# Kernel tuning notes

Measured on AMD Instinct MI355X. Metric: run time of the kernel, lower is better.

## Reference

```python
import jax, jax.numpy as jnp
import numpy as np

B, CIN, L = 16, 256, 2048
HID, G, M = 512, 2, 512
LP = L // 2  # pooled length == hidden_length of patterns
BETA = 1.0


def setup_inputs() -> dict:
    key = jax.random.key(0)
    k = jax.random.split(key, 6)
    x = jax.random.normal(k[0], (B, CIN, L), dtype=jnp.float32)
    # ChannelPool: Conv1d(256 -> 512, kernel=1, groups=2): weight [512, 128, 1]
    w1 = jax.random.normal(k[1], (HID, CIN // G, 1), dtype=jnp.float32) * 0.05
    b1 = jax.random.normal(k[2], (HID,), dtype=jnp.float32) * 0.01
    # StatePattern memory bank: [num_memories, hidden_length]
    patterns = jax.random.normal(k[3], (M, LP), dtype=jnp.float32) * 0.02
    # Unpool: ConvTranspose1d(512 -> 256, kernel=2, stride=2, groups=2):
    # torch weight layout [in_channels, out_channels//groups, kernel] = [512, 128, 2]
    wT = jax.random.normal(k[4], (HID, CIN // G, 2), dtype=jnp.float32) * 0.05
    bT = jax.random.normal(k[5], (CIN,), dtype=jnp.float32) * 0.01
    RZ = jnp.array(0.1, dtype=jnp.float32)
    return {"x": x, "w1": w1, "b1": b1, "patterns": patterns, "wT": wT, "bT": bT, "RZ": RZ}


def reference(x, w1, b1, patterns, wT, bT, RZ):
    identity = x
    # --- grouped 1x1 conv (ChannelPool) ---
    # split channels into G groups: x [B,G,CIN/G,L], w [G,HID/G,CIN/G]
    xg = x.reshape(B, G, CIN // G, L)
    wg = w1[:, :, 0].reshape(G, HID // G, CIN // G)
    h = jnp.einsum('bgil,goi->bgol', xg, wg).reshape(B, HID, L) + b1[None, :, None]
    h = jax.nn.relu(h)  # act; norm1/dropout are identity (norm=False, eval)
    # --- MaxPool1d(kernel=2, stride=2) ---
    h = h.reshape(B, HID, LP, 2).max(axis=-1)  # [B, HID, LP]
    # --- Hopfield retrieval: softmax(beta * x @ P^T) @ P ---
    scores = jnp.einsum('bcl,ml->bcm', BETA * h, patterns)  # [B, HID, M]
    attn = jax.nn.softmax(scores, axis=-1)
    h = jnp.einsum('bcm,ml->bcl', attn, patterns)  # [B, HID, LP]
    # --- grouped ConvTranspose1d(k=2, s=2) ---
    hg = h.reshape(B, G, HID // G, LP)
    wtg = wT.reshape(G, HID // G, CIN // G, 2)
    y = jnp.einsum('bgil,giok->bgolk', hg, wtg)  # [B,G,CIN/G,LP,2]
    y = y.reshape(B, CIN, L) + bT[None, :, None]
    y = jax.nn.relu(y)  # act; norm2/dropout identity
    return identity + RZ * y
```

## Files before the change

kernel.cpp:

```cpp
#include <hip/hip_runtime.h>

#define NB 16
#define NCIN 256
#define NL 2048
#define NHID 512
#define NM 512
#define NLP 1024

typedef short bf16x8 __attribute__((ext_vector_type(8)));
typedef unsigned short u16x8 __attribute__((ext_vector_type(8)));
typedef float f32x4 __attribute__((ext_vector_type(4)));
typedef __attribute__((address_space(1))) const unsigned int gas_u32;
typedef __attribute__((address_space(3))) unsigned int las_u32;

__device__ __forceinline__ unsigned short f2bf(float f) {
    unsigned int u = __builtin_bit_cast(unsigned int, f);
    return (unsigned short)((u + 0x7FFFu + ((u >> 16) & 1u)) >> 16);
}
__device__ __forceinline__ float bf2f(unsigned short u) {
    return __builtin_bit_cast(float, ((unsigned int)u) << 16);
}

__global__ __launch_bounds__(512) void k_front(
    const float* __restrict__ x, const float* __restrict__ w1,
    const float* __restrict__ b1, const float* __restrict__ P,
    const float* __restrict__ wT, unsigned short* __restrict__ hb,
    unsigned short* __restrict__ Pb, unsigned short* __restrict__ Ptb,
    unsigned short* __restrict__ wTt)
{
    __shared__ __align__(16) unsigned short smem[66560];
    const int bb = blockIdx.x;
    const int t = threadIdx.x;

    if (bb >= 512) {
        if (bb < 640) {
            unsigned short (*tbuf)[65] = (unsigned short (*)[65])smem;
            const int pb = bb - 512;
            const int mt = pb >> 4, lt = pb & 15;
            for (int i = t; i < 4096; i += 512) {
                const int r = i >> 6, c = i & 63;
                const unsigned short v = f2bf(P[(size_t)(mt * 64 + r) * 1024 + lt * 64 + c]);
                Pb[(size_t)(mt * 64 + r) * 1024 + lt * 64 + c] = v;
                tbuf[c][r] = v;
            }
            __syncthreads();
            for (int i = t; i < 4096; i += 512) {
                const int r = i >> 6, c = i & 63;
                Ptb[(size_t)(lt * 64 + r) * 512 + mt * 64 + c] = tbuf[r][c];
            }
        } else {
            const int t5 = (bb - 640) * 512 + t;
            const int g = t5 >> 16, ok = (t5 >> 8) & 255, i = t5 & 255;
            wTt[t5] = f2bf(wT[(size_t)(g * 256 + i) * 256 + ok]);
        }
        return;
    }

    const int g  = bb & 1;
    const int rt = bb >> 1;
    const int r0 = rt * 128;
    const int b  = r0 >> 11, l0 = r0 & 2047;

    unsigned short* T   = smem;
    unsigned short* Asl = smem + 17408;
    unsigned short* Bsl = smem + 33792;
    unsigned short* epi = smem;

    #pragma unroll
    for (int i3 = 0; i3 < 8; ++i3) {
        const int idx = i3 * 512 + t;
        const int ch = idx >> 5, f4 = idx & 31;
        const float4 v = *(const float4*)(x + ((size_t)(b * 256 + g * 128 + ch)) * 2048 + l0 + f4 * 4);
        ushort4 u;
        u.x = f2bf(v.x); u.y = f2bf(v.y); u.z = f2bf(v.z); u.w = f2bf(v.w);
        *(ushort4*)(T + ch * 136 + f4 * 4) = u;
    }
    #pragma unroll
    for (int i5 = 0; i5 < 16; ++i5) {
        const int idx = i5 * 512 + t;
        const int o = idx >> 5, f4 = idx & 31;
        const float4 v = *(const float4*)(w1 + ((size_t)(g * 256 + o)) * 128 + f4 * 4);
        ushort4 u;
        u.x = f2bf(v.x); u.y = f2bf(v.y); u.z = f2bf(v.z); u.w = f2bf(v.w);
        *(ushort4*)(Bsl + o * 128 + f4 * 4) = u;
    }
    __syncthreads();
    #pragma unroll
    for (int i4 = 0; i4 < 4; ++i4) {
        const int idx = i4 * 512 + t;
        const int ch = idx & 127, lo = idx >> 7;
        const u16x8 v = *(const u16x8*)(T + ch * 136 + lo * 8);
        #pragma unroll
        for (int u2 = 0; u2 < 8; ++u2)
            Asl[(lo * 8 + u2) * 128 + ch] = v[u2];
    }
    __syncthreads();

    const int lane = t & 63, wave = t >> 6;
    const int wm = wave & 1, wn = wave >> 1;
    const int q = lane >> 4, lm = lane & 15;

    f32x4 acc[4][4];
    #pragma unroll
    for (int i = 0; i < 4; ++i)
        #pragma unroll
        for (int j = 0; j < 4; ++j)
            #pragma unroll
            for (int r = 0; r < 4; ++r) acc[i][j][r] = 0.f;

    #pragma unroll
    for (int kc = 0; kc < 4; ++kc) {
        bf16x8 af[4], bf[4];
        #pragma unroll
        for (int i = 0; i < 4; ++i)
            af[i] = *(const bf16x8*)(Asl + (wm * 64 + i * 16 + lm) * 128 + kc * 32 + q * 8);
        #pragma unroll
        for (int j = 0; j < 4; ++j)
            bf[j] = *(const bf16x8*)(Bsl + (wn * 64 + j * 16 + lm) * 128 + kc * 32 + q * 8);
        #pragma unroll
        for (int i = 0; i < 4; ++i)
            #pragma unroll
            for (int j = 0; j < 4; ++j)
                acc[i][j] = __builtin_amdgcn_mfma_f32_16x16x32_bf16(af[i], bf[j], acc[i][j], 0, 0, 0);
    }
    __syncthreads();

    #pragma unroll
    for (int j = 0; j < 4; ++j) {
        const int col = wn * 64 + j * 16 + lm;
        const float bias = b1[g * 256 + col];
        #pragma unroll
        for (int i = 0; i < 4; ++i) {
            const float p0 = fmaxf(fmaxf(acc[i][j][0], acc[i][j][1]) + bias, 0.f);
            const float p1 = fmaxf(fmaxf(acc[i][j][2], acc[i][j][3]) + bias, 0.f);
            const int lp_loc = wm * 32 + i * 8 + q * 2;
            ushort2 u; u.x = f2bf(p0); u.y = f2bf(p1);
            *(ushort2*)(epi + col * 72 + lp_loc) = u;
        }
    }
    __syncthreads();
    const int c_loc = t >> 1, half = t & 1;
    unsigned short* dst = hb + ((size_t)(b * 512 + g * 256 + c_loc)) * 1024 + (l0 >> 1) + half * 32;
    #pragma unroll
    for (int u = 0; u < 4; ++u)
        *(u16x8*)(dst + u * 8) = *(const u16x8*)(epi + c_loc * 72 + half * 32 + u * 8);
}

__global__ __launch_bounds__(512) void k_hop(
    const unsigned short* __restrict__ hb, const unsigned short* __restrict__ Pb,
    const unsigned short* __restrict__ Ptb, unsigned short* __restrict__ h2T)
{
    __shared__ __align__(16) unsigned short smem[51712];
    unsigned short* Sbuf = smem;
    unsigned short* Asl  = smem + 16896;
    unsigned short* Bsl  = smem + 16896 + 2048;
    unsigned short* Bsl2 = smem + 16896;

    const int t = threadIdx.x;
    const int r0 = blockIdx.x * 32;
    const int b = r0 >> 9, c0 = r0 & 511;
    const int lane = t & 63, wave = t >> 6;
    const int q = lane >> 4, lm = lane & 15;

    f32x4 acc1[2][4];
    #pragma unroll
    for (int i = 0; i < 2; ++i)
        #pragma unroll
        for (int j = 0; j < 4; ++j)
            #pragma unroll
            for (int r = 0; r < 4; ++r) acc1[i][j][r] = 0.f;

    for (int kc0 = 0; kc0 < 1024; kc0 += 64) {
        if (t < 256) {
            const int e = t * 8;
            const int row = e >> 6, col = e & 63;
            const unsigned short* ga = hb + (size_t)(r0 + row) * 1024 + kc0 + col;
            __builtin_amdgcn_global_load_lds((gas_u32*)ga, (las_u32*)(Asl + e), 16, 0, 0);
        }
        #pragma unroll
        for (int i2 = 0; i2 < 8; ++i2) {
            const int e = (i2 * 512 + t) * 8;
            const int row = e >> 6, col = e & 63;
            const unsigned short* gb = Pb + (size_t)row * 1024 + kc0 + col;
            __builtin_amdgcn_global_load_lds((gas_u32*)gb, (las_u32*)(Bsl + e), 16, 0, 0);
        }
        __syncthreads();
        #pragma unroll
        for (int kk = 0; kk < 2; ++kk) {
            bf16x8 af[2], bf[4];
            #pragma unroll
            for (int i = 0; i < 2; ++i)
                af[i] = *(const bf16x8*)(Asl + (i * 16 + lm) * 64 + kk * 32 + q * 8);
            #pragma unroll
            for (int j = 0; j < 4; ++j)
                bf[j] = *(const bf16x8*)(Bsl + (wave * 64 + j * 16 + lm) * 64 + kk * 32 + q * 8);
            #pragma unroll
            for (int i = 0; i < 2; ++i)
                #pragma unroll
                for (int j = 0; j < 4; ++j)
                    acc1[i][j] = __builtin_amdgcn_mfma_f32_16x16x32_bf16(af[i], bf[j], acc1[i][j], 0, 0, 0);
        }
        __syncthreads();
    }

    #pragma unroll
    for (int i = 0; i < 2; ++i)
        #pragma unroll
        for (int j = 0; j < 4; ++j)
            #pragma unroll
            for (int r = 0; r < 4; ++r)
                Sbuf[(i * 16 + q * 4 + r) * 528 + wave * 64 + j * 16 + lm] = f2bf(acc1[i][j][r]);
    __syncthreads();

    {
        const int rw = t >> 4, sl = t & 15;
        u16x8 sv[4];
        #pragma unroll
        for (int u = 0; u < 4; ++u)
            sv[u] = *(const u16x8*)(Sbuf + rw * 528 + sl * 32 + u * 8);
        float mx = -3.0e38f;
        #pragma unroll
        for (int u = 0; u < 4; ++u)
            #pragma unroll
            for (int j = 0; j < 8; ++j) mx = fmaxf(mx, bf2f(sv[u][j]));
        #pragma unroll
        for (int off = 1; off < 16; off <<= 1) mx = fmaxf(mx, __shfl_xor(mx, off));
        float vv[32];
        float sum = 0.f;
        #pragma unroll
        for (int u = 0; u < 4; ++u)
            #pragma unroll
            for (int j = 0; j < 8; ++j) {
                const float e = __expf(bf2f(sv[u][j]) - mx);
                vv[u * 8 + j] = e; sum += e;
            }
        #pragma unroll
        for (int off = 1; off < 16; off <<= 1) sum += __shfl_xor(sum, off);
        const float inv = 1.f / sum;
        #pragma unroll
        for (int u = 0; u < 4; ++u) {
            u16x8 ov;
            #pragma unroll
            for (int j = 0; j < 8; ++j) ov[j] = f2bf(vv[u * 8 + j] * inv);
            *(u16x8*)(Sbuf + rw * 528 + sl * 32 + u * 8) = ov;
        }
    }
    __syncthreads();

    bf16x8 a[2][16];
    #pragma unroll
    for (int i = 0; i < 2; ++i)
        #pragma unroll
        for (int kx = 0; kx < 16; ++kx)
            a[i][kx] = *(const bf16x8*)(Sbuf + (i * 16 + lm) * 528 + kx * 32 + q * 8);

    for (int lpc = 0; lpc < 4; ++lpc) {
        const int lp0c = lpc * 256;
        f32x4 acc2[2][2];
        #pragma unroll
        for (int i = 0; i < 2; ++i)
            #pragma unroll
            for (int j = 0; j < 2; ++j)
                #pragma unroll
                for (int r = 0; r < 4; ++r) acc2[i][j][r] = 0.f;

        for (int kc0 = 0; kc0 < 4; ++kc0) {
            #pragma unroll
            for (int i2 = 0; i2 < 8; ++i2) {
                const int e = (i2 * 512 + t) * 8;
                const int row = e >> 7, col = e & 127;
                const unsigned short* gb = Ptb + (size_t)(lp0c + row) * 512 + kc0 * 128 + col;
                __builtin_amdgcn_global_load_lds((gas_u32*)gb, (las_u32*)(Bsl2 + e), 16, 0, 0);
            }
            __syncthreads();
            #pragma unroll
            for (int kk = 0; kk < 4; ++kk) {
                const int kx = kc0 * 4 + kk;
                bf16x8 bf2[2];
                #pragma unroll
                for (int j = 0; j < 2; ++j)
                    bf2[j] = *(const bf16x8*)(Bsl2 + (wave * 32 + j * 16 + lm) * 128 + kk * 32 + q * 8);
                #pragma unroll
                for (int i = 0; i < 2; ++i)
                    #pragma unroll
                    for (int j = 0; j < 2; ++j)
                        acc2[i][j] = __builtin_amdgcn_mfma_f32_16x16x32_bf16(a[i][kx], bf2[j], acc2[i][j], 0, 0, 0);
            }
            __syncthreads();
        }
        #pragma unroll
        for (int i = 0; i < 2; ++i)
            #pragma unroll
            for (int j = 0; j < 2; ++j) {
                const int lp = lp0c + wave * 32 + j * 16 + lm;
                ushort4 u;
                u.x = f2bf(acc2[i][j][0]); u.y = f2bf(acc2[i][j][1]);
                u.z = f2bf(acc2[i][j][2]); u.w = f2bf(acc2[i][j][3]);
                *(ushort4*)(h2T + ((size_t)b * 1024 + lp) * 512 + c0 + i * 16 + q * 4) = u;
            }
    }
}

__global__ __launch_bounds__(256) void k4_gemm(
    const unsigned short* __restrict__ h2T, const unsigned short* __restrict__ wTt,
    const float* __restrict__ bT, const float* __restrict__ x,
    const float* __restrict__ RZ, float* __restrict__ out)
{
    const int nt = blockIdx.x & 1;
    const int g  = (blockIdx.x >> 1) & 1;
    const int rt = blockIdx.x >> 2;
    const int r0 = rt * 128;
    const int b  = r0 >> 10, lp0 = r0 & 1023;

    __shared__ __align__(16) char smem[65536];
    unsigned short* Asl = (unsigned short*)smem;
    unsigned short* Bsl = Asl + 128 * 64;
    float* epi = (float*)smem;

    const int t = threadIdx.x;
    const int lane = t & 63;
    const int wave = t >> 6;
    const int wm = wave & 1, wn = wave >> 1;
    const int q = lane >> 4, lm = lane & 15;

    f32x4 acc[4][4];
    #pragma unroll
    for (int i = 0; i < 4; ++i)
        #pragma unroll
        for (int j = 0; j < 4; ++j)
            #pragma unroll
            for (int r = 0; r < 4; ++r) acc[i][j][r] = 0.f;

    for (int k0 = 0; k0 < 256; k0 += 64) {
        #pragma unroll
        for (int rd = 0; rd < 4; ++rd) {
            const int e = rd * 2048 + t * 8;
            const int row = e >> 6, col = e & 63;
            const unsigned short* ga = h2T + (size_t)(r0 + row) * 512 + g * 256 + k0 + col;
            __builtin_amdgcn_global_load_lds((gas_u32*)ga, (las_u32*)(Asl + e), 16, 0, 0);
            const unsigned short* gb = wTt + (size_t)g * 65536 + (size_t)(nt * 128 + row) * 256 + k0 + col;
            __builtin_amdgcn_global_load_lds((gas_u32*)gb, (las_u32*)(Bsl + e), 16, 0, 0);
        }
        __syncthreads();
        #pragma unroll
        for (int kk = 0; kk < 2; ++kk) {
            bf16x8 af[4], bf[4];
            #pragma unroll
            for (int i = 0; i < 4; ++i)
                af[i] = *(const bf16x8*)(Asl + (wm * 64 + i * 16 + lm) * 64 + kk * 32 + q * 8);
            #pragma unroll
            for (int j = 0; j < 4; ++j)
                bf[j] = *(const bf16x8*)(Bsl + (wn * 64 + j * 16 + lm) * 64 + kk * 32 + q * 8);
            #pragma unroll
            for (int i = 0; i < 4; ++i)
                #pragma unroll
                for (int j = 0; j < 4; ++j)
                    acc[i][j] = __builtin_amdgcn_mfma_f32_16x16x32_bf16(af[i], bf[j], acc[i][j], 0, 0, 0);
        }
        __syncthreads();
    }

    #pragma unroll
    for (int j = 0; j < 4; ++j) {
        const int col_blk = wn * 64 + j * 16 + lm;
        const int o_l = col_blk >> 1, kk2 = col_blk & 1;
        #pragma unroll
        for (int i = 0; i < 4; ++i) {
            #pragma unroll
            for (int r = 0; r < 4; ++r) {
                const int row_l = wm * 64 + i * 16 + q * 4 + r;
                const int l_l = 2 * row_l + kk2;
                const int chunk = ((l_l >> 2) + o_l) & 63;
                epi[o_l * 256 + chunk * 4 + (l_l & 3)] = acc[i][j][r];
            }
        }
    }
    __syncthreads();
    const int row = t >> 2, quad = t & 3;
    const int c = g * 128 + nt * 64 + row;
    const float bias = bT[c];
    const float rz = RZ[0];
    const size_t gbase = ((size_t)(b * 256 + c)) * 2048 + 2 * lp0 + quad * 64;
    #pragma unroll
    for (int k = 0; k < 16; ++k) {
        const int chunk_phys = (quad * 16 + k + row) & 63;
        const float4 v = *(const float4*)(epi + row * 256 + chunk_phys * 4);
        const float4 xv = *(const float4*)(x + gbase + k * 4);
        float4 o;
        o.x = xv.x + rz * fmaxf(v.x + bias, 0.f);
        o.y = xv.y + rz * fmaxf(v.y + bias, 0.f);
        o.z = xv.z + rz * fmaxf(v.z + bias, 0.f);
        o.w = xv.w + rz * fmaxf(v.w + bias, 0.f);
        *(float4*)(out + gbase + k * 4) = o;
    }
}

extern "C" void kernel_launch(void* const* d_in, const int* in_sizes, int n_in,
                              void* d_out, int out_size, void* d_ws, size_t ws_size,
                              hipStream_t stream) {
    (void)in_sizes; (void)n_in; (void)out_size; (void)ws_size;
    const float* x  = (const float*)d_in[0];
    const float* w1 = (const float*)d_in[1];
    const float* b1 = (const float*)d_in[2];
    const float* P  = (const float*)d_in[3];
    const float* wT = (const float*)d_in[4];
    const float* bT = (const float*)d_in[5];
    const float* RZ = (const float*)d_in[6];
    float* out = (float*)d_out;

    char* ws = (char*)d_ws;
    unsigned short* hb  = (unsigned short*)ws;
    unsigned short* h2T = (unsigned short*)(ws + (16u << 20));
    unsigned short* Pb  = (unsigned short*)(ws + (32u << 20));
    unsigned short* Ptb = (unsigned short*)(ws + (33u << 20));
    unsigned short* wTt = (unsigned short*)(ws + (34u << 20));

    hipLaunchKernelGGL(k_front, dim3(896), dim3(512), 0, stream,
                       x, w1, b1, P, wT, hb, Pb, Ptb, wTt);
    hipLaunchKernelGGL(k_hop,   dim3(256), dim3(512), 0, stream, hb, Pb, Ptb, h2T);
    hipLaunchKernelGGL(k4_gemm, dim3(512), dim3(256), 0, stream, h2T, wTt, bT, x, RZ, out);
}
```

Measured before the change: 201.2 us.

## Split fused Hopfield kernel into score GEMM and softmax-fused retrieval GEMM

```diff
diff --git a/kernel.cpp b/kernel.cpp
--- a/kernel.cpp
+++ b/kernel.cpp
@@ -146,159 +146,165 @@
         *(u16x8*)(dst + u * 8) = *(const u16x8*)(epi + c_loc * 72 + half * 32 + u * 8);
 }
 
-__global__ __launch_bounds__(512) void k_hop(
-    const unsigned short* __restrict__ hb, const unsigned short* __restrict__ Pb,
-    const unsigned short* __restrict__ Ptb, unsigned short* __restrict__ h2T)
+__global__ __launch_bounds__(512, 2) void gemm_sc(
+    const unsigned short* __restrict__ A, const unsigned short* __restrict__ B,
+    unsigned short* __restrict__ Sb)
 {
-    __shared__ __align__(16) unsigned short smem[51712];
-    unsigned short* Sbuf = smem;
-    unsigned short* Asl  = smem + 16896;
-    unsigned short* Bsl  = smem + 16896 + 2048;
-    unsigned short* Bsl2 = smem + 16896;
+    const int nt = blockIdx.x & 3;
+    const int rt = blockIdx.x >> 2;
+    const int r0 = rt * 128, n0 = nt * 128;
+
+    __shared__ unsigned short Asl[128 * 64];
+    __shared__ unsigned short Bsl[128 * 64];
 
     const int t = threadIdx.x;
-    const int r0 = blockIdx.x * 32;
-    const int b = r0 >> 9, c0 = r0 & 511;
-    const int lane = t & 63, wave = t >> 6;
+    const int lane = t & 63;
+    const int wave = t >> 6;
+    const int wm = wave & 1, wn = wave >> 1;
     const int q = lane >> 4, lm = lane & 15;
 
-    f32x4 acc1[2][4];
-    #pragma unroll
-    for (int i = 0; i < 2; ++i)
-        #pragma unroll
-        for (int j = 0; j < 4; ++j)
-            #pragma unroll
-            for (int r = 0; r < 4; ++r) acc1[i][j][r] = 0.f;
-
-    for (int kc0 = 0; kc0 < 1024; kc0 += 64) {
-        if (t < 256) {
-            const int e = t * 8;
+    f32x4 acc[4][2];
+    #pragma unroll
+    for (int i = 0; i < 4; ++i)
+        #pragma unroll
+        for (int j = 0; j < 2; ++j)
+            #pragma unroll
+            for (int r = 0; r < 4; ++r) acc[i][j][r] = 0.f;
+
+    for (int k0 = 0; k0 < 1024; k0 += 64) {
+        #pragma unroll
+        for (int rd = 0; rd < 2; ++rd) {
+            const int e = rd * 4096 + t * 8;
             const int row = e >> 6, col = e & 63;
-            const unsigned short* ga = hb + (size_t)(r0 + row) * 1024 + kc0 + col;
+            const unsigned short* ga = A + (size_t)(r0 + row) * 1024 + k0 + col;
             __builtin_amdgcn_global_load_lds((gas_u32*)ga, (las_u32*)(Asl + e), 16, 0, 0);
-        }
-        #pragma unroll
-        for (int i2 = 0; i2 < 8; ++i2) {
-            const int e = (i2 * 512 + t) * 8;
-            const int row = e >> 6, col = e & 63;
-            const unsigned short* gb = Pb + (size_t)row * 1024 + kc0 + col;
+            const unsigned short* gb = B + (size_t)(n0 + row) * 1024 + k0 + col;
             __builtin_amdgcn_global_load_lds((gas_u32*)gb, (las_u32*)(Bsl + e), 16, 0, 0);
         }
         __syncthreads();
         #pragma unroll
         for (int kk = 0; kk < 2; ++kk) {
-            bf16x8 af[2], bf[4];
-            #pragma unroll
-            for (int i = 0; i < 2; ++i)
-                af[i] = *(const bf16x8*)(Asl + (i * 16 + lm) * 64 + kk * 32 + q * 8);
-            #pragma unroll
-            for (int j = 0; j < 4; ++j)
-                bf[j] = *(const bf16x8*)(Bsl + (wave * 64 + j * 16 + lm) * 64 + kk * 32 + q * 8);
-            #pragma unroll
-            for (int i = 0; i < 2; ++i)
-                #pragma unroll
-                for (int j = 0; j < 4; ++j)
-                    acc1[i][j] = __builtin_amdgcn_mfma_f32_16x16x32_bf16(af[i], bf[j], acc1[i][j], 0, 0, 0);
-        }
-        __syncthreads();
-    }
-
-    #pragma unroll
-    for (int i = 0; i < 2; ++i)
-        #pragma unroll
-        for (int j = 0; j < 4; ++j)
-            #pragma unroll
-            for (int r = 0; r < 4; ++r)
-                Sbuf[(i * 16 + q * 4 + r) * 528 + wave * 64 + j * 16 + lm] = f2bf(acc1[i][j][r]);
-    __syncthreads();
-
-    {
-        const int rw = t >> 4, sl = t & 15;
-        u16x8 sv[4];
-        #pragma unroll
-        for (int u = 0; u < 4; ++u)
-            sv[u] = *(const u16x8*)(Sbuf + rw * 528 + sl * 32 + u * 8);
-        float mx = -3.0e38f;
-        #pragma unroll
-        for (int u = 0; u < 4; ++u)
-            #pragma unroll
-            for (int j = 0; j < 8; ++j) mx = fmaxf(mx, bf2f(sv[u][j]));
-        #pragma unroll
-        for (int off = 1; off < 16; off <<= 1) mx = fmaxf(mx, __shfl_xor(mx, off));
-        float vv[32];
-        float sum = 0.f;
-        #pragma unroll
-        for (int u = 0; u < 4; ++u)
-            #pragma unroll
-            for (int j = 0; j < 8; ++j) {
-                const float e = __expf(bf2f(sv[u][j]) - mx);
-                vv[u * 8 + j] = e; sum += e;
-            }
-        #pragma unroll
-        for (int off = 1; off < 16; off <<= 1) sum += __shfl_xor(sum, off);
-        const float inv = 1.f / sum;
-        #pragma unroll
-        for (int u = 0; u < 4; ++u) {
-            u16x8 ov;
-            #pragma unroll
-            for (int j = 0; j < 8; ++j) ov[j] = f2bf(vv[u * 8 + j] * inv);
-            *(u16x8*)(Sbuf + rw * 528 + sl * 32 + u * 8) = ov;
-        }
-    }
-    __syncthreads();
-
-    bf16x8 a[2][16];
-    #pragma unroll
-    for (int i = 0; i < 2; ++i)
-        #pragma unroll
-        for (int kx = 0; kx < 16; ++kx)
-            a[i][kx] = *(const bf16x8*)(Sbuf + (i * 16 + lm) * 528 + kx * 32 + q * 8);
-
-    for (int lpc = 0; lpc < 4; ++lpc) {
-        const int lp0c = lpc * 256;
-        f32x4 acc2[2][2];
-        #pragma unroll
-        for (int i = 0; i < 2; ++i)
+            bf16x8 af[4], bf[2];
+            #pragma unroll
+            for (int i = 0; i < 4; ++i)
+                af[i] = *(const bf16x8*)(Asl + (wm * 64 + i * 16 + lm) * 64 + kk * 32 + q * 8);
             #pragma unroll
             for (int j = 0; j < 2; ++j)
-                #pragma unroll
-                for (int r = 0; r < 4; ++r) acc2[i][j][r] = 0.f;
-
-        for (int kc0 = 0; kc0 < 4; ++kc0) {
-            #pragma unroll
-            for (int i2 = 0; i2 < 8; ++i2) {
-                const int e = (i2 * 512 + t) * 8;
-                const int row = e >> 7, col = e & 127;
-                const unsigned short* gb = Ptb + (size_t)(lp0c + row) * 512 + kc0 * 128 + col;
-                __builtin_amdgcn_global_load_lds((gas_u32*)gb, (las_u32*)(Bsl2 + e), 16, 0, 0);
-            }
-            __syncthreads();
-            #pragma unroll
-            for (int kk = 0; kk < 4; ++kk) {
-                const int kx = kc0 * 4 + kk;
-                bf16x8 bf2[2];
+                bf[j] = *(const bf16x8*)(Bsl + (wn * 32 + j * 16 + lm) * 64 + kk * 32 + q * 8);
+            #pragma unroll
+            for (int i = 0; i < 4; ++i)
                 #pragma unroll
                 for (int j = 0; j < 2; ++j)
-                    bf2[j] = *(const bf16x8*)(Bsl2 + (wave * 32 + j * 16 + lm) * 128 + kk * 32 + q * 8);
+                    acc[i][j] = __builtin_amdgcn_mfma_f32_16x16x32_bf16(af[i], bf[j], acc[i][j], 0, 0, 0);
+        }
+        __syncthreads();
+    }
+
+    #pragma unroll
+    for (int i = 0; i < 4; ++i)
+        #pragma unroll
+        for (int j = 0; j < 2; ++j)
+            #pragma unroll
+            for (int r = 0; r < 4; ++r)
+                Sb[(size_t)(r0 + wm * 64 + i * 16 + q * 4 + r) * 512
+                   + n0 + wn * 32 + j * 16 + lm] = f2bf(acc[i][j][r]);
+}
+
+__global__ __launch_bounds__(512, 2) void gemm_retr_sm(
+    const unsigned short* __restrict__ Ptb, const unsigned short* __restrict__ Sb,
+    unsigned short* __restrict__ h2T)
+{
+    const int tl = blockIdx.x & 31;
+    const int b  = blockIdx.x >> 5;
+    const int nt = tl & 3;
+    const int rt = tl >> 2;
+    const int r0 = rt * 128, n0 = nt * 128;
+
+    __shared__ unsigned short Asl[128 * 64];
+    __shared__ unsigned short Bsl[128 * 64];
+    __shared__ float Mrow[128];
+    __shared__ float Inv[128];
+
+    const int t = threadIdx.x;
+    const int lane = t & 63;
+    const int wave = t >> 6;
+    const int wm = wave & 1, wn = wave >> 1;
+    const int q = lane >> 4, lm = lane & 15;
+
+    {
+        const int row = t >> 2, part = t & 3;
+        const unsigned short* srow = Sb + ((size_t)b * 512 + n0 + row) * 512 + part * 128;
+        float mx = -3.0e38f;
+        #pragma unroll
+        for (int u = 0; u < 16; ++u) {
+            const u16x8 v = *(const u16x8*)(srow + u * 8);
+            #pragma unroll
+            for (int j = 0; j < 8; ++j) mx = fmaxf(mx, bf2f(v[j]));
+        }
+        mx = fmaxf(mx, __shfl_xor(mx, 1));
+        mx = fmaxf(mx, __shfl_xor(mx, 2));
+        float sum = 0.f;
+        #pragma unroll
+        for (int u = 0; u < 16; ++u) {
+            const u16x8 v = *(const u16x8*)(srow + u * 8);
+            #pragma unroll
+            for (int j = 0; j < 8; ++j) sum += __expf(bf2f(v[j]) - mx);
+        }
+        sum += __shfl_xor(sum, 1);
+        sum += __shfl_xor(sum, 2);
+        if (part == 0) { Mrow[row] = mx; Inv[row] = 1.f / sum; }
+    }
+    __syncthreads();
+
+    f32x4 acc[4][2];
+    #pragma unroll
+    for (int i = 0; i < 4; ++i)
+        #pragma unroll
+        for (int j = 0; j < 2; ++j)
+            #pragma unroll
+            for (int r = 0; r < 4; ++r) acc[i][j][r] = 0.f;
+
+    for (int k0 = 0; k0 < 512; k0 += 64) {
+        #pragma unroll
+        for (int rd = 0; rd < 2; ++rd) {
+            const int e = rd * 4096 + t * 8;
+            const int row = e >> 6, col = e & 63;
+            const unsigned short* ga = Ptb + (size_t)(r0 + row) * 512 + k0 + col;
+            __builtin_amdgcn_global_load_lds((gas_u32*)ga, (las_u32*)(Asl + e), 16, 0, 0);
+            const u16x8 sv = *(const u16x8*)(Sb + ((size_t)b * 512 + n0 + row) * 512 + k0 + col);
+            const float m = Mrow[row], inv = Inv[row];
+            u16x8 ov;
+            #pragma unroll
+            for (int j = 0; j < 8; ++j) ov[j] = f2bf(__expf(bf2f(sv[j]) - m) * inv);
+            *(u16x8*)(Bsl + e) = ov;
+        }
+        __syncthreads();
+        #pragma unroll
+        for (int kk = 0; kk < 2; ++kk) {
+            bf16x8 af[4], bf[2];
+            #pragma unroll
+            for (int i = 0; i < 4; ++i)
+                af[i] = *(const bf16x8*)(Asl + (wm * 64 + i * 16 + lm) * 64 + kk * 32 + q * 8);
+            #pragma unroll
+            for (int j = 0; j < 2; ++j)
+                bf[j] = *(const bf16x8*)(Bsl + (wn * 32 + j * 16 + lm) * 64 + kk * 32 + q * 8);
+            #pragma unroll
+            for (int i = 0; i < 4; ++i)
                 #pragma unroll
-                for (int i = 0; i < 2; ++i)
-                    #pragma unroll
-                    for (int j = 0; j < 2; ++j)
-                        acc2[i][j] = __builtin_amdgcn_mfma_f32_16x16x32_bf16(a[i][kx], bf2[j], acc2[i][j], 0, 0, 0);
-            }
-            __syncthreads();
-        }
-        #pragma unroll
-        for (int i = 0; i < 2; ++i)
-            #pragma unroll
-            for (int j = 0; j < 2; ++j) {
-                const int lp = lp0c + wave * 32 + j * 16 + lm;
-                ushort4 u;
-                u.x = f2bf(acc2[i][j][0]); u.y = f2bf(acc2[i][j][1]);
-                u.z = f2bf(acc2[i][j][2]); u.w = f2bf(acc2[i][j][3]);
-                *(ushort4*)(h2T + ((size_t)b * 1024 + lp) * 512 + c0 + i * 16 + q * 4) = u;
-            }
-    }
+                for (int j = 0; j < 2; ++j)
+                    acc[i][j] = __builtin_amdgcn_mfma_f32_16x16x32_bf16(af[i], bf[j], acc[i][j], 0, 0, 0);
+        }
+        __syncthreads();
+    }
+
+    #pragma unroll
+    for (int i = 0; i < 4; ++i)
+        #pragma unroll
+        for (int j = 0; j < 2; ++j)
+            #pragma unroll
+            for (int r = 0; r < 4; ++r)
+                h2T[((size_t)b * 1024 + r0 + wm * 64 + i * 16 + q * 4 + r) * 512
+                    + n0 + wn * 32 + j * 16 + lm] = f2bf(acc[i][j][r]);
 }
 
 __global__ __launch_bounds__(256) void k4_gemm(
@@ -414,9 +420,11 @@
     unsigned short* Pb  = (unsigned short*)(ws + (32u << 20));
     unsigned short* Ptb = (unsigned short*)(ws + (33u << 20));
     unsigned short* wTt = (unsigned short*)(ws + (34u << 20));
-
-    hipLaunchKernelGGL(k_front, dim3(896), dim3(512), 0, stream,
+    unsigned short* Sb  = (unsigned short*)out;
+
+    hipLaunchKernelGGL(k_front,      dim3(896), dim3(512), 0, stream,
                        x, w1, b1, P, wT, hb, Pb, Ptb, wTt);
-    hipLaunchKernelGGL(k_hop,   dim3(256), dim3(512), 0, stream, hb, Pb, Ptb, h2T);
-    hipLaunchKernelGGL(k4_gemm, dim3(512), dim3(256), 0, stream, h2T, wTt, bT, x, RZ, out);
-}
+    hipLaunchKernelGGL(gemm_sc,      dim3(256), dim3(512), 0, stream, hb, Pb, Sb);
+    hipLaunchKernelGGL(gemm_retr_sm, dim3(512), dim3(512), 0, stream, Ptb, Sb, h2T);
+    hipLaunchKernelGGL(k4_gemm,      dim3(512), dim3(256), 0, stream, h2T, wTt, bT, x, RZ, out);
+}
```

Result: no change. 204.3 us (+1.5%).
